# Performance work log

Measured on AMD Instinct MI355X. Metric: run time of the kernel, lower is better.

Reference implementation:

```python
import jax, jax.numpy as jnp
import numpy as np

N_NODES = 20000
N_EDGES = 160000
IN_DIM = 512
HID = 256
N_CLASSES = 2
NUM_GRAPHS = 16


def setup_inputs() -> dict:
    key = jax.random.key(0)
    ks = jax.random.split(key, 12)
    x = jax.random.normal(ks[0], (N_NODES, IN_DIM), dtype=jnp.float32)
    edge_index = jax.random.randint(ks[1], (2, N_EDGES), 0, N_NODES, dtype=jnp.int64)
    batch = jnp.sort(jax.random.randint(ks[2], (N_NODES,), 0, NUM_GRAPHS, dtype=jnp.int64))
    def glorot(k, shape):
        lim = float(np.sqrt(6.0 / (shape[0] + shape[1])))
        return jax.random.uniform(k, shape, jnp.float32, -lim, lim)
    return {
        "x": x,
        "edge_index": edge_index,
        "batch": batch,
        "W1n": glorot(ks[3], (IN_DIM, HID)),
        "W1s": glorot(ks[4], (IN_DIM, HID)),
        "b1": jnp.zeros((HID,), jnp.float32),
        "W2n": glorot(ks[5], (HID, HID)),
        "W2s": glorot(ks[6], (HID, HID)),
        "b2": jnp.zeros((HID,), jnp.float32),
        "fc1w": glorot(ks[7], (HID, HID // 2)),
        "fc1b": jnp.zeros((HID // 2,), jnp.float32),
        "fc2w": glorot(ks[8], (HID // 2, N_CLASSES)),
        "fc2b": jnp.zeros((N_CLASSES,), jnp.float32),
    }


def _sage_conv(x, W_nbr, W_self, b, src, dst, n_nodes):
    # mean-aggregate neighbor features (messages flow src -> dst, PyG convention)
    deg = jax.ops.segment_sum(jnp.ones(src.shape, x.dtype), dst, num_segments=n_nodes)
    deg = jnp.maximum(deg, 1.0)
    aggr = jax.ops.segment_sum(x[src], dst, num_segments=n_nodes) / deg[:, None]
    # SAGEConv: lin_l(aggr) + lin_r(x) + bias (equivalent to concat-linear)
    return aggr @ W_nbr + x @ W_self + b


def reference(x, edge_index, batch, W1n, W1s, b1, W2n, W2s, b2, fc1w, fc1b, fc2w, fc2b):
    src, dst = edge_index[0], edge_index[1]
    n = x.shape[0]
    h = jax.nn.relu(_sage_conv(x, W1n, W1s, b1, src, dst, n))
    h = jax.nn.relu(_sage_conv(h, W2n, W2s, b2, src, dst, n))
    # global_mean_pool over graph ids
    cnt = jax.ops.segment_sum(jnp.ones((n,), h.dtype), batch, num_segments=NUM_GRAPHS)
    pooled = jax.ops.segment_sum(h, batch, num_segments=NUM_GRAPHS) / jnp.maximum(cnt, 1.0)[:, None]
    out = jax.nn.relu(pooled @ fc1w + fc1b) @ fc2w + fc2b
    return out
```

## Files before the change

### kernel.cpp

```cpp
#include <hip/hip_runtime.h>
#include <hip/hip_bf16.h>


#define HID 256
#define NCOL 512

typedef __bf16 bf16x8 __attribute__((ext_vector_type(8)));
typedef float floatx4 __attribute__((ext_vector_type(4)));
typedef unsigned int u32;
typedef const u32 __attribute__((address_space(1)))* gp_t;
typedef u32 __attribute__((address_space(3)))* lp_t;

__device__ __forceinline__ ushort f2bf(float f) {
    unsigned u = __float_as_uint(f);
    u += 0x7fffu + ((u >> 16) & 1u);
    return (ushort)(u >> 16);
}
__device__ __forceinline__ float bf2f(ushort b) {
    return __uint_as_float(((unsigned)b) << 16);
}

__device__ __forceinline__ void packT_work(const float* __restrict__ Wn,
                                           const float* __restrict__ Ws,
                                           ushort* __restrict__ WT, int K, int gid) {
    if (gid >= NCOL * K) return;
    int n = gid / K, k = gid - n * K;
    float v = (n < HID) ? Wn[k * HID + n] : Ws[k * HID + (n - HID)];
    WT[gid] = f2bf(v);
}

__global__ void prep_kernel(const float* __restrict__ x, ushort* __restrict__ xb, int n4,
                            const float* __restrict__ W1n, const float* __restrict__ W1s,
                            ushort* __restrict__ w1t, int K1,
                            const float* __restrict__ W2n, const float* __restrict__ W2s,
                            ushort* __restrict__ w2t, int K2,
                            const int* __restrict__ dst, int* __restrict__ degi, int n_edges,
                            int nb_cvt, int nb_w1, int nb_w2) {
    int bx = blockIdx.x, t = threadIdx.x;
    if (bx < nb_cvt) {
        int i = bx * 256 + t;
        if (i < n4) {
            float4 v = ((const float4*)x)[i];
            ushort4 o;
            o.x = f2bf(v.x); o.y = f2bf(v.y); o.z = f2bf(v.z); o.w = f2bf(v.w);
            ((ushort4*)xb)[i] = o;
        }
    } else if (bx < nb_cvt + nb_w1) {
        packT_work(W1n, W1s, w1t, K1, (bx - nb_cvt) * 256 + t);
    } else if (bx < nb_cvt + nb_w1 + nb_w2) {
        packT_work(W2n, W2s, w2t, K2, (bx - nb_cvt - nb_w1) * 256 + t);
    } else {
        int e = (bx - nb_cvt - nb_w1 - nb_w2) * 256 + t;
        if (e < n_edges) atomicAdd(&degi[dst[e]], 1);
    }
}

__global__ __launch_bounds__(256) void psum_kernel(const int* __restrict__ degi,
                                                   int* __restrict__ partials, int n) {
    int t = threadIdx.x;
    int i = blockIdx.x * 256 + t;
    int v = (i < n) ? degi[i] : 0;
#pragma unroll
    for (int d = 1; d < 64; d <<= 1) v += __shfl_xor(v, d, 64);
    __shared__ int wsum[4];
    if ((t & 63) == 0) wsum[t >> 6] = v;
    __syncthreads();
    if (t == 0) partials[blockIdx.x] = wsum[0] + wsum[1] + wsum[2] + wsum[3];
}

__global__ __launch_bounds__(256) void scan2_kernel(const int* __restrict__ degi,
                                                    const int* __restrict__ partials,
                                                    int* __restrict__ off,
                                                    int* __restrict__ cursor, int n, int nb) {
    int t = threadIdx.x, lane = t & 63, w = t >> 6;
    int c = blockIdx.x;
    int pre = 0, tot = 0;
    for (int base = 0; base < nb; base += 64) {
        int idx = base + lane;
        int pv = (idx < nb) ? partials[idx] : 0;
        pre += (idx < c) ? pv : 0;
        tot += pv;
    }
#pragma unroll
    for (int d = 1; d < 64; d <<= 1) {
        pre += __shfl_xor(pre, d, 64);
        tot += __shfl_xor(tot, d, 64);
    }
    if (c == 0 && t == 0) off[n] = tot;
    int i = c * 256 + t;
    int v = (i < n) ? degi[i] : 0;
    int s = v;
#pragma unroll
    for (int d = 1; d < 64; d <<= 1) {
        int u = __shfl_up(s, d, 64);
        if (lane >= d) s += u;
    }
    __shared__ int wsum[4];
    if (lane == 63) wsum[w] = s;
    __syncthreads();
    int woff = 0;
    for (int k = 0; k < w; ++k) woff += wsum[k];
    int excl = pre + woff + s - v;
    if (i < n) { off[i] = excl; cursor[i] = excl; }
}

__global__ void fill_kernel(const int* __restrict__ src, const int* __restrict__ dst,
                            int* __restrict__ cursor, int* __restrict__ eidx, int n_edges) {
    int e = blockIdx.x * 256 + threadIdx.x;
    if (e < n_edges) {
        int p = atomicAdd(&cursor[dst[e]], 1);
        eidx[p] = src[e];
    }
}

__global__ __launch_bounds__(256) void gemm_mfma(const ushort* __restrict__ A,
                                                 const ushort* __restrict__ BT,
                                                 ushort* __restrict__ Y, int K, int nG) {
    int b = blockIdx.x;
    int xcd = b & 7, rest = b >> 3;
    int m = rest & 3, Ggrp = rest >> 2;
    int G = xcd + 8 * Ggrp;
    if (G >= nG) return;
    int m0 = G * 64, n0 = m * 128;

    __shared__ ushort As[2][64 * 64];
    __shared__ ushort Bs[2][128 * 64];
    int tid = threadIdx.x;
    int w = tid >> 6, lane = tid & 63;
    int quad = lane >> 4, r16 = lane & 15;
    int wm = (w >> 1) * 32, wn = (w & 1) * 64;

    int arow[2], agu[2], brow[4], bgu[4];
#pragma unroll
    for (int rr = 0; rr < 2; ++rr) {
        int idx = rr * 256 + tid;
        arow[rr] = idx >> 3;
        agu[rr] = (idx & 7) ^ (arow[rr] & 7);
    }
#pragma unroll
    for (int rr = 0; rr < 4; ++rr) {
        int idx = rr * 256 + tid;
        brow[rr] = idx >> 3;
        bgu[rr] = (idx & 7) ^ (brow[rr] & 7);
    }

    auto stage = [&](int buf, int k0) {
#pragma unroll
        for (int rr = 0; rr < 2; ++rr) {
            const ushort* ga = A + (size_t)(m0 + arow[rr]) * K + k0 + agu[rr] * 8;
            ushort* la = As[buf] + (size_t)(rr * 256 + w * 64) * 8;
            __builtin_amdgcn_global_load_lds((gp_t)(const void*)ga, (lp_t)(void*)la, 16, 0, 0);
        }
#pragma unroll
        for (int rr = 0; rr < 4; ++rr) {
            const ushort* gb = BT + (size_t)(n0 + brow[rr]) * K + k0 + bgu[rr] * 8;
            ushort* lb = Bs[buf] + (size_t)(rr * 256 + w * 64) * 8;
            __builtin_amdgcn_global_load_lds((gp_t)(const void*)gb, (lp_t)(void*)lb, 16, 0, 0);
        }
    };

    floatx4 acc[2][4];
#pragma unroll
    for (int i = 0; i < 2; ++i)
#pragma unroll
        for (int j = 0; j < 4; ++j) acc[i][j] = (floatx4){0.f, 0.f, 0.f, 0.f};

    const int nk = K >> 6;
    stage(0, 0);
    for (int t = 0; t < nk; ++t) {
        int cb = t & 1;
        __syncthreads();
        if (t + 1 < nk) stage(cb ^ 1, (t + 1) << 6);
        const ushort* Ab = As[cb];
        const ushort* Bb = Bs[cb];
#pragma unroll
        for (int s = 0; s < 2; ++s) {
            bf16x8 a[2], b2[4];
#pragma unroll
            for (int i = 0; i < 2; ++i) {
                int row = wm + i * 16 + r16;
                int au = (s * 4 + quad) ^ (row & 7);
                a[i] = *(const bf16x8*)(Ab + row * 64 + au * 8);
            }
#pragma unroll
            for (int j = 0; j < 4; ++j) {
                int row = wn + j * 16 + r16;
                int bu = (s * 4 + quad) ^ (row & 7);
                b2[j] = *(const bf16x8*)(Bb + row * 64 + bu * 8);
            }
#pragma unroll
            for (int i = 0; i < 2; ++i)
#pragma unroll
                for (int j = 0; j < 4; ++j)
                    acc[i][j] = __builtin_amdgcn_mfma_f32_16x16x32_bf16(a[i], b2[j], acc[i][j], 0, 0, 0);
        }
    }
#pragma unroll
    for (int i = 0; i < 2; ++i)
#pragma unroll
        for (int j = 0; j < 4; ++j) {
            int col = n0 + wn + j * 16 + r16;
#pragma unroll
            for (int rg = 0; rg < 4; ++rg) {
                int row = m0 + wm + i * 16 + quad * 4 + rg;
                Y[(size_t)row * NCOL + col] = f2bf(acc[i][j][rg]);
            }
        }
}

#define ACC4(A, Yv) { A.x += bf2f(Yv.x); A.y += bf2f(Yv.y); A.z += bf2f(Yv.z); A.w += bf2f(Yv.w); }
__global__ __launch_bounds__(256) void gather_kernel(const ushort* __restrict__ Y,
                                                     const int* __restrict__ off,
                                                     const int* __restrict__ eidx,
                                                     const float* __restrict__ bias,
                                                     ushort* __restrict__ h, int n_nodes) {
    int tid = threadIdx.x;
    int v = blockIdx.x * 4 + (tid >> 6);
    if (v >= n_nodes) return;
    int lane = tid & 63;
    int q4 = lane << 2;
    int e0 = off[v], e1 = off[v + 1];
    ushort4 sv = *(const ushort4*)(Y + (size_t)v * NCOL + HID + q4);
    float4 b = *(const float4*)(bias + q4);
    float4 a0 = make_float4(0.f, 0.f, 0.f, 0.f), a1 = a0, a2 = a0, a3 = a0;
    for (int base = e0; base < e1; base += 64) {
        int ecnt = min(64, e1 - base);
        int ev = (lane < ecnt) ? eidx[base + lane] : 0;
        int j = 0;
        for (; j + 8 <= ecnt; j += 8) {
            int s0 = __shfl(ev, j + 0), s1 = __shfl(ev, j + 1);
            int s2 = __shfl(ev, j + 2), s3 = __shfl(ev, j + 3);
            int s4 = __shfl(ev, j + 4), s5 = __shfl(ev, j + 5);
            int s6 = __shfl(ev, j + 6), s7 = __shfl(ev, j + 7);
            ushort4 y0 = *(const ushort4*)(Y + (size_t)s0 * NCOL + q4);
            ushort4 y1 = *(const ushort4*)(Y + (size_t)s1 * NCOL + q4);
            ushort4 y2 = *(const ushort4*)(Y + (size_t)s2 * NCOL + q4);
            ushort4 y3 = *(const ushort4*)(Y + (size_t)s3 * NCOL + q4);
            ushort4 y4 = *(const ushort4*)(Y + (size_t)s4 * NCOL + q4);
            ushort4 y5 = *(const ushort4*)(Y + (size_t)s5 * NCOL + q4);
            ushort4 y6 = *(const ushort4*)(Y + (size_t)s6 * NCOL + q4);
            ushort4 y7 = *(const ushort4*)(Y + (size_t)s7 * NCOL + q4);
            ACC4(a0, y0); ACC4(a1, y1); ACC4(a2, y2); ACC4(a3, y3);
            ACC4(a0, y4); ACC4(a1, y5); ACC4(a2, y6); ACC4(a3, y7);
        }
        for (; j < ecnt; ++j) {
            int s = __shfl(ev, j);
            ushort4 y = *(const ushort4*)(Y + (size_t)s * NCOL + q4);
            ACC4(a0, y);
        }
    }
    float invd = 1.0f / fmaxf((float)(e1 - e0), 1.0f);
    ushort4 r;
    r.x = f2bf(fmaxf((a0.x + a1.x + a2.x + a3.x) * invd + bf2f(sv.x) + b.x, 0.f));
    r.y = f2bf(fmaxf((a0.y + a1.y + a2.y + a3.y) * invd + bf2f(sv.y) + b.y, 0.f));
    r.z = f2bf(fmaxf((a0.z + a1.z + a2.z + a3.z) * invd + bf2f(sv.z) + b.z, 0.f));
    r.w = f2bf(fmaxf((a0.w + a1.w + a2.w + a3.w) * invd + bf2f(sv.w) + b.w, 0.f));
    *(ushort4*)(h + (size_t)v * HID + q4) = r;
}

__global__ void pool_kernel(const ushort* __restrict__ h, const int* __restrict__ batch,
                            float* __restrict__ pooled, float* __restrict__ cnt, int n_nodes) {
    int f = threadIdx.x;
    int v0 = blockIdx.x * 64;
    int vend = min(v0 + 64, n_nodes);
    if (v0 >= n_nodes) return;
    int cur = batch[v0];
    float acc = 0.f, ac = 0.f;
    for (int v = v0; v < vend; ++v) {
        int g = batch[v];
        if (g != cur) {
            atomicAdd(&pooled[cur * HID + f], acc);
            if (f == 0) atomicAdd(&cnt[cur], ac);
            acc = 0.f; ac = 0.f; cur = g;
        }
        acc += bf2f(h[(size_t)v * HID + f]);
        ac += 1.0f;
    }
    atomicAdd(&pooled[cur * HID + f], acc);
    if (f == 0) atomicAdd(&cnt[cur], ac);
}

__global__ void head_kernel(const float* __restrict__ pooled, const float* __restrict__ cnt,
                            const float* __restrict__ fc1w, const float* __restrict__ fc1b,
                            const float* __restrict__ fc2w, const float* __restrict__ fc2b,
                            float* __restrict__ out) {
    int g = blockIdx.x, j = threadIdx.x;
    __shared__ float p[256];
    __shared__ float hid[128];
    float inv = 1.0f / fmaxf(cnt[g], 1.0f);
    p[j] = pooled[g * HID + j] * inv;
    p[j + 128] = pooled[g * HID + 128 + j] * inv;
    __syncthreads();
    float a = fc1b[j];
    for (int f = 0; f < 256; ++f) a += p[f] * fc1w[f * 128 + j];
    hid[j] = fmaxf(a, 0.f);
    __syncthreads();
    if (j < 2) {
        float o = fc2b[j];
        for (int t = 0; t < 128; ++t) o += hid[t] * fc2w[t * 2 + j];
        out[g * 2 + j] = o;
    }
}

extern "C" void kernel_launch(void* const* d_in, const int* in_sizes, int n_in,
                              void* d_out, int out_size, void* d_ws, size_t ws_size,
                              hipStream_t stream) {
    const float* x    = (const float*)d_in[0];
    const int*   ei   = (const int*)d_in[1];
    const int*   batch= (const int*)d_in[2];
    const float* W1n  = (const float*)d_in[3];
    const float* W1s  = (const float*)d_in[4];
    const float* b1   = (const float*)d_in[5];
    const float* W2n  = (const float*)d_in[6];
    const float* W2s  = (const float*)d_in[7];
    const float* b2   = (const float*)d_in[8];
    const float* fc1w = (const float*)d_in[9];
    const float* fc1b = (const float*)d_in[10];
    const float* fc2w = (const float*)d_in[11];
    const float* fc2b = (const float*)d_in[12];
    float* out = (float*)d_out;

    const int n_nodes = in_sizes[2];
    const int n_edges = in_sizes[1] / 2;
    const int in_dim  = in_sizes[0] / n_nodes;
    const int Mpad    = (n_nodes + 63) & ~63;
    const int nb      = (n_nodes + 255) / 256;
    const int nG      = Mpad / 64;
    const int* src = ei;
    const int* dst = ei + n_edges;

    char* wsb = (char*)d_ws;
    size_t cur = 0;
    auto alloc = [&](size_t nbytes) { size_t o = cur; cur = (cur + nbytes + 255) & ~(size_t)255; return o; };
    size_t o_degi = alloc((size_t)n_nodes * 4);
    size_t o_off  = alloc((size_t)(n_nodes + 1) * 4);
    size_t o_cur  = alloc((size_t)n_nodes * 4);
    size_t o_part = alloc((size_t)nb * 4);
    size_t o_eidx = alloc((size_t)n_edges * 4);
    size_t o_w1   = alloc((size_t)NCOL * in_dim * 2);
    size_t o_w2   = alloc((size_t)NCOL * HID * 2);
    size_t o_xb   = alloc((size_t)Mpad * in_dim * 2);
    size_t o_hb   = alloc((size_t)Mpad * HID * 2);
    size_t o_y    = alloc((size_t)Mpad * NCOL * 2);
    size_t o_pool = alloc((size_t)16 * HID * 4 + 16 * 4);
    (void)ws_size;

    int*    degi    = (int*)(wsb + o_degi);
    int*    off     = (int*)(wsb + o_off);
    int*    cursor  = (int*)(wsb + o_cur);
    int*    partials= (int*)(wsb + o_part);
    int*    eidx    = (int*)(wsb + o_eidx);
    ushort* w1t     = (ushort*)(wsb + o_w1);
    ushort* w2t     = (ushort*)(wsb + o_w2);
    ushort* xb      = (ushort*)(wsb + o_xb);
    ushort* hb      = (ushort*)(wsb + o_hb);
    ushort* Y       = (ushort*)(wsb + o_y);
    float*  pooled  = (float*)(wsb + o_pool);
    float*  cnt     = pooled + 16 * HID;

    hipMemsetAsync(degi, 0, (size_t)n_nodes * 4, stream);
    hipMemsetAsync(pooled, 0, (size_t)(16 * HID + 16) * 4, stream);

    int n4 = n_nodes * in_dim / 4;
    int nb_cvt = (n4 + 255) / 256;
    int nb_w1  = (NCOL * in_dim + 255) / 256;
    int nb_w2  = (NCOL * HID + 255) / 256;
    int nb_deg = (n_edges + 255) / 256;
    prep_kernel<<<nb_cvt + nb_w1 + nb_w2 + nb_deg, 256, 0, stream>>>(
        x, xb, n4, W1n, W1s, w1t, in_dim, W2n, W2s, w2t, HID,
        dst, degi, n_edges, nb_cvt, nb_w1, nb_w2);

    psum_kernel<<<nb, 256, 0, stream>>>(degi, partials, n_nodes);
    scan2_kernel<<<nb, 256, 0, stream>>>(degi, partials, off, cursor, n_nodes, nb);
    fill_kernel<<<(n_edges + 255) / 256, 256, 0, stream>>>(src, dst, cursor, eidx, n_edges);

    int gemm_blocks = 8 * 4 * ((nG + 7) / 8);
    int gather_blocks = (n_nodes + 3) / 4;

    gemm_mfma<<<gemm_blocks, 256, 0, stream>>>(xb, w1t, Y, in_dim, nG);
    gather_kernel<<<gather_blocks, 256, 0, stream>>>(Y, off, eidx, b1, hb, n_nodes);

    gemm_mfma<<<gemm_blocks, 256, 0, stream>>>(hb, w2t, Y, HID, nG);
    gather_kernel<<<gather_blocks, 256, 0, stream>>>(Y, off, eidx, b2, hb, n_nodes);

    pool_kernel<<<(n_nodes + 63) / 64, 256, 0, stream>>>(hb, batch, pooled, cnt, n_nodes);
    head_kernel<<<16, 128, 0, stream>>>(pooled, cnt, fc1w, fc1b, fc2w, fc2b, out);
}
```

Baseline: 223.4 us.

## Split GEMM output into neighbor and self buffers, fuse pool and head

The GEMM output is split into two 256-column buffers, one for the neighbor projection and one for the self projection, in place of one interleaved 512-column buffer. Gather then reads compact 512-byte rows, which should pack more useful neighbor data per cache line and in L2. The pool and head kernels are merged with a last-block ticket, and the two memsets become one, removing a launch and a memset. The fused head runs serially in a single block over all 16 graphs.

```diff
diff --git a/kernel.cpp b/kernel.cpp
--- a/kernel.cpp
+++ b/kernel.cpp
@@ -115,7 +115,8 @@
 
 __global__ __launch_bounds__(256) void gemm_mfma(const ushort* __restrict__ A,
                                                  const ushort* __restrict__ BT,
-                                                 ushort* __restrict__ Y, int K, int nG) {
+                                                 ushort* __restrict__ Ynb,
+                                                 ushort* __restrict__ Ysb, int K, int nG) {
     int b = blockIdx.x;
     int xcd = b & 7, rest = b >> 3;
     int m = rest & 3, Ggrp = rest >> 2;
@@ -195,21 +196,24 @@
                     acc[i][j] = __builtin_amdgcn_mfma_f32_16x16x32_bf16(a[i], b2[j], acc[i][j], 0, 0, 0);
         }
     }
+    ushort* out = (n0 < HID) ? Ynb : Ysb;
+    int nbase = n0 & (HID - 1);
 #pragma unroll
     for (int i = 0; i < 2; ++i)
 #pragma unroll
         for (int j = 0; j < 4; ++j) {
-            int col = n0 + wn + j * 16 + r16;
+            int col = nbase + wn + j * 16 + r16;
 #pragma unroll
             for (int rg = 0; rg < 4; ++rg) {
                 int row = m0 + wm + i * 16 + quad * 4 + rg;
-                Y[(size_t)row * NCOL + col] = f2bf(acc[i][j][rg]);
+                out[(size_t)row * HID + col] = f2bf(acc[i][j][rg]);
             }
         }
 }
 
 #define ACC4(A, Yv) { A.x += bf2f(Yv.x); A.y += bf2f(Yv.y); A.z += bf2f(Yv.z); A.w += bf2f(Yv.w); }
-__global__ __launch_bounds__(256) void gather_kernel(const ushort* __restrict__ Y,
+__global__ __launch_bounds__(256) void gather_kernel(const ushort* __restrict__ Ynb,
+                                                     const ushort* __restrict__ Ysb,
                                                      const int* __restrict__ off,
                                                      const int* __restrict__ eidx,
                                                      const float* __restrict__ bias,
@@ -220,7 +224,7 @@
     int lane = tid & 63;
     int q4 = lane << 2;
     int e0 = off[v], e1 = off[v + 1];
-    ushort4 sv = *(const ushort4*)(Y + (size_t)v * NCOL + HID + q4);
+    ushort4 sv = *(const ushort4*)(Ysb + (size_t)v * HID + q4);
     float4 b = *(const float4*)(bias + q4);
     float4 a0 = make_float4(0.f, 0.f, 0.f, 0.f), a1 = a0, a2 = a0, a3 = a0;
     for (int base = e0; base < e1; base += 64) {
@@ -232,20 +236,20 @@
             int s2 = __shfl(ev, j + 2), s3 = __shfl(ev, j + 3);
             int s4 = __shfl(ev, j + 4), s5 = __shfl(ev, j + 5);
             int s6 = __shfl(ev, j + 6), s7 = __shfl(ev, j + 7);
-            ushort4 y0 = *(const ushort4*)(Y + (size_t)s0 * NCOL + q4);
-            ushort4 y1 = *(const ushort4*)(Y + (size_t)s1 * NCOL + q4);
-            ushort4 y2 = *(const ushort4*)(Y + (size_t)s2 * NCOL + q4);
-            ushort4 y3 = *(const ushort4*)(Y + (size_t)s3 * NCOL + q4);
-            ushort4 y4 = *(const ushort4*)(Y + (size_t)s4 * NCOL + q4);
-            ushort4 y5 = *(const ushort4*)(Y + (size_t)s5 * NCOL + q4);
-            ushort4 y6 = *(const ushort4*)(Y + (size_t)s6 * NCOL + q4);
-            ushort4 y7 = *(const ushort4*)(Y + (size_t)s7 * NCOL + q4);
+            ushort4 y0 = *(const ushort4*)(Ynb + (size_t)s0 * HID + q4);
+            ushort4 y1 = *(const ushort4*)(Ynb + (size_t)s1 * HID + q4);
+            ushort4 y2 = *(const ushort4*)(Ynb + (size_t)s2 * HID + q4);
+            ushort4 y3 = *(const ushort4*)(Ynb + (size_t)s3 * HID + q4);
+            ushort4 y4 = *(const ushort4*)(Ynb + (size_t)s4 * HID + q4);
+            ushort4 y5 = *(const ushort4*)(Ynb + (size_t)s5 * HID + q4);
+            ushort4 y6 = *(const ushort4*)(Ynb + (size_t)s6 * HID + q4);
+            ushort4 y7 = *(const ushort4*)(Ynb + (size_t)s7 * HID + q4);
             ACC4(a0, y0); ACC4(a1, y1); ACC4(a2, y2); ACC4(a3, y3);
             ACC4(a0, y4); ACC4(a1, y5); ACC4(a2, y6); ACC4(a3, y7);
         }
         for (; j < ecnt; ++j) {
             int s = __shfl(ev, j);
-            ushort4 y = *(const ushort4*)(Y + (size_t)s * NCOL + q4);
+            ushort4 y = *(const ushort4*)(Ynb + (size_t)s * HID + q4);
             ACC4(a0, y);
         }
     }
@@ -258,47 +262,55 @@
     *(ushort4*)(h + (size_t)v * HID + q4) = r;
 }
 
-__global__ void pool_kernel(const ushort* __restrict__ h, const int* __restrict__ batch,
-                            float* __restrict__ pooled, float* __restrict__ cnt, int n_nodes) {
+__global__ __launch_bounds__(256) void pool_head_kernel(
+        const ushort* __restrict__ h, const int* __restrict__ batch,
+        float* __restrict__ pooled, float* __restrict__ cnt, int* __restrict__ ticket,
+        const float* __restrict__ fc1w, const float* __restrict__ fc1b,
+        const float* __restrict__ fc2w, const float* __restrict__ fc2b,
+        float* __restrict__ out, int n_nodes) {
     int f = threadIdx.x;
     int v0 = blockIdx.x * 64;
     int vend = min(v0 + 64, n_nodes);
-    if (v0 >= n_nodes) return;
-    int cur = batch[v0];
-    float acc = 0.f, ac = 0.f;
-    for (int v = v0; v < vend; ++v) {
-        int g = batch[v];
-        if (g != cur) {
-            atomicAdd(&pooled[cur * HID + f], acc);
-            if (f == 0) atomicAdd(&cnt[cur], ac);
-            acc = 0.f; ac = 0.f; cur = g;
-        }
-        acc += bf2f(h[(size_t)v * HID + f]);
-        ac += 1.0f;
-    }
-    atomicAdd(&pooled[cur * HID + f], acc);
-    if (f == 0) atomicAdd(&cnt[cur], ac);
-}
-
-__global__ void head_kernel(const float* __restrict__ pooled, const float* __restrict__ cnt,
-                            const float* __restrict__ fc1w, const float* __restrict__ fc1b,
-                            const float* __restrict__ fc2w, const float* __restrict__ fc2b,
-                            float* __restrict__ out) {
-    int g = blockIdx.x, j = threadIdx.x;
+    if (v0 < n_nodes) {
+        int cur = batch[v0];
+        float acc = 0.f, ac = 0.f;
+        for (int v = v0; v < vend; ++v) {
+            int g = batch[v];
+            if (g != cur) {
+                atomicAdd(&pooled[cur * HID + f], acc);
+                if (f == 0) atomicAdd(&cnt[cur], ac);
+                acc = 0.f; ac = 0.f; cur = g;
+            }
+            acc += bf2f(h[(size_t)v * HID + f]);
+            ac += 1.0f;
+        }
+        atomicAdd(&pooled[cur * HID + f], acc);
+        if (f == 0) atomicAdd(&cnt[cur], ac);
+    }
+    __threadfence();
+    __shared__ int done;
+    if (f == 0) done = atomicAdd(ticket, 1);
+    __syncthreads();
+    if (done != (int)gridDim.x - 1) return;
+    __threadfence();
     __shared__ float p[256];
-    __shared__ float hid[128];
-    float inv = 1.0f / fmaxf(cnt[g], 1.0f);
-    p[j] = pooled[g * HID + j] * inv;
-    p[j + 128] = pooled[g * HID + 128 + j] * inv;
-    __syncthreads();
-    float a = fc1b[j];
-    for (int f = 0; f < 256; ++f) a += p[f] * fc1w[f * 128 + j];
-    hid[j] = fmaxf(a, 0.f);
-    __syncthreads();
-    if (j < 2) {
-        float o = fc2b[j];
-        for (int t = 0; t < 128; ++t) o += hid[t] * fc2w[t * 2 + j];
-        out[g * 2 + j] = o;
+    __shared__ float hidv[128];
+    for (int g = 0; g < 16; ++g) {
+        float inv = 1.0f / fmaxf(cnt[g], 1.0f);
+        p[f] = pooled[g * HID + f] * inv;
+        __syncthreads();
+        if (f < 128) {
+            float a = fc1b[f];
+            for (int k = 0; k < 256; ++k) a += p[k] * fc1w[k * 128 + f];
+            hidv[f] = fmaxf(a, 0.f);
+        }
+        __syncthreads();
+        if (f < 2) {
+            float o = fc2b[f];
+            for (int k = 0; k < 128; ++k) o += hidv[k] * fc2w[k * 2 + f];
+            out[g * 2 + f] = o;
+        }
+        __syncthreads();
     }
 }
 
@@ -332,7 +344,8 @@
     char* wsb = (char*)d_ws;
     size_t cur = 0;
     auto alloc = [&](size_t nbytes) { size_t o = cur; cur = (cur + nbytes + 255) & ~(size_t)255; return o; };
-    size_t o_degi = alloc((size_t)n_nodes * 4);
+    size_t zero_bytes = (size_t)n_nodes * 4 + (size_t)16 * HID * 4 + 16 * 4 + 4;
+    size_t o_zero = alloc(zero_bytes);
     size_t o_off  = alloc((size_t)(n_nodes + 1) * 4);
     size_t o_cur  = alloc((size_t)n_nodes * 4);
     size_t o_part = alloc((size_t)nb * 4);
@@ -341,11 +354,14 @@
     size_t o_w2   = alloc((size_t)NCOL * HID * 2);
     size_t o_xb   = alloc((size_t)Mpad * in_dim * 2);
     size_t o_hb   = alloc((size_t)Mpad * HID * 2);
-    size_t o_y    = alloc((size_t)Mpad * NCOL * 2);
-    size_t o_pool = alloc((size_t)16 * HID * 4 + 16 * 4);
+    size_t o_yn   = alloc((size_t)Mpad * HID * 2);
+    size_t o_ys   = alloc((size_t)Mpad * HID * 2);
     (void)ws_size;
 
-    int*    degi    = (int*)(wsb + o_degi);
+    int*    degi    = (int*)(wsb + o_zero);
+    float*  pooled  = (float*)(wsb + o_zero + (size_t)n_nodes * 4);
+    float*  cnt     = pooled + 16 * HID;
+    int*    ticket  = (int*)(cnt + 16);
     int*    off     = (int*)(wsb + o_off);
     int*    cursor  = (int*)(wsb + o_cur);
     int*    partials= (int*)(wsb + o_part);
@@ -354,12 +370,10 @@
     ushort* w2t     = (ushort*)(wsb + o_w2);
     ushort* xb      = (ushort*)(wsb + o_xb);
     ushort* hb      = (ushort*)(wsb + o_hb);
-    ushort* Y       = (ushort*)(wsb + o_y);
-    float*  pooled  = (float*)(wsb + o_pool);
-    float*  cnt     = pooled + 16 * HID;
-
-    hipMemsetAsync(degi, 0, (size_t)n_nodes * 4, stream);
-    hipMemsetAsync(pooled, 0, (size_t)(16 * HID + 16) * 4, stream);
+    ushort* Ynb     = (ushort*)(wsb + o_yn);
+    ushort* Ysb     = (ushort*)(wsb + o_ys);
+
+    hipMemsetAsync(degi, 0, zero_bytes, stream);
 
     int n4 = n_nodes * in_dim / 4;
     int nb_cvt = (n4 + 255) / 256;
@@ -377,12 +391,12 @@
     int gemm_blocks = 8 * 4 * ((nG + 7) / 8);
     int gather_blocks = (n_nodes + 3) / 4;
 
-    gemm_mfma<<<gemm_blocks, 256, 0, stream>>>(xb, w1t, Y, in_dim, nG);
-    gather_kernel<<<gather_blocks, 256, 0, stream>>>(Y, off, eidx, b1, hb, n_nodes);
-
-    gemm_mfma<<<gemm_blocks, 256, 0, stream>>>(hb, w2t, Y, HID, nG);
-    gather_kernel<<<gather_blocks, 256, 0, stream>>>(Y, off, eidx, b2, hb, n_nodes);
-
-    pool_kernel<<<(n_nodes + 63) / 64, 256, 0, stream>>>(hb, batch, pooled, cnt, n_nodes);
-    head_kernel<<<16, 128, 0, stream>>>(pooled, cnt, fc1w, fc1b, fc2w, fc2b, out);
-}
+    gemm_mfma<<<gemm_blocks, 256, 0, stream>>>(xb, w1t, Ynb, Ysb, in_dim, nG);
+    gather_kernel<<<gather_blocks, 256, 0, stream>>>(Ynb, Ysb, off, eidx, b1, hb, n_nodes);
+
+    gemm_mfma<<<gemm_blocks, 256, 0, stream>>>(hb, w2t, Ynb, Ysb, HID, nG);
+    gather_kernel<<<gather_blocks, 256, 0, stream>>>(Ynb, Ysb, off, eidx, b2, hb, n_nodes);
+
+    pool_head_kernel<<<(n_nodes + 63) / 64, 256, 0, stream>>>(
+        hb, batch, pooled, cnt, ticket, fc1w, fc1b, fc2w, fc2b, out, n_nodes);
+}
```

Result: slower. 300.3 us (+34.4%).
